# Kernel optimization log

Measured on AMD Instinct MI355X. Metric: run time of the kernel, lower is better.

Reference implementation:

```python
import jax, jax.numpy as jnp
import numpy as np

N_NODES = 100000
N_EDGES = 3200000
D_IN = 512
D_OUT = 256


def setup_inputs() -> dict:
    key = jax.random.key(0)
    k1, k2, k3, k4, k5 = jax.random.split(key, 5)
    x = jax.random.normal(k1, (N_NODES, D_IN), dtype=jnp.float32)
    edge_row = jax.random.randint(k2, (N_EDGES,), 0, N_NODES, dtype=jnp.int32)
    edge_col = jax.random.randint(k3, (N_EDGES,), 0, N_NODES, dtype=jnp.int32)
    edge_vals = jax.random.uniform(k4, (N_EDGES,), dtype=jnp.float32)
    # glorot uniform for W, zeros for bias (as in the torch module)
    init_range = float(np.sqrt(6.0 / (D_IN + D_OUT)))
    W = jax.random.uniform(k5, (D_IN, D_OUT), minval=-init_range, maxval=init_range, dtype=jnp.float32)
    b = jnp.zeros((D_OUT,), dtype=jnp.float32)
    return {"x": x, "edge_row": edge_row, "edge_col": edge_col,
            "edge_vals": edge_vals, "W": W, "b": b}


def reference(x, edge_row, edge_col, edge_vals, W, b):
    # dropout p=0 -> identity; feature transform
    pre_sup = x @ W                                   # [N, D_OUT]
    # SpMM: out[i] = sum_{e: row[e]==i} vals[e] * pre_sup[col[e]]
    gathered = pre_sup[edge_col] * edge_vals[:, None]  # [E, D_OUT]
    agg = jax.ops.segment_sum(gathered, edge_row, num_segments=N_NODES)
    out = agg + b
    # F.normalize(p=2, dim=0): L2-normalize each column over the node dim
    col_norm = jnp.sqrt(jnp.sum(out * out, axis=0, keepdims=True))
    out = out / jnp.maximum(col_norm, 1e-12)
    return jax.nn.softplus(out)
```

## Files before the change

### kernel.cpp

```cpp
#include <hip/hip_runtime.h>
#include <math.h>

#define N_NODES 100000
#define N_EDGES 3200000
#define D_IN 512
#define D_OUT 256
#define NBUK 391
#define LDA 40
#define NREP 8

typedef unsigned short ushort_t;
typedef unsigned int uint_t;

using f32x4 = __attribute__((ext_vector_type(4))) float;
using s16x8 = __attribute__((ext_vector_type(8))) short;
using u32x4 = __attribute__((ext_vector_type(4))) uint_t;

__device__ __forceinline__ ushort_t f2bf(float f) {
    union { float f; uint_t u; } v; v.f = f;
    uint_t r = v.u + 0x7FFFu + ((v.u >> 16) & 1u);
    return (ushort_t)(r >> 16);
}
__device__ __forceinline__ float bf2f(uint_t u) {
    union { uint_t u; float f; } v; v.u = u << 16;
    return v.f;
}

__global__ __launch_bounds__(256) void cvt_w(const float* __restrict__ W,
                                             ushort_t* __restrict__ Wt) {
    int idx = blockIdx.x * 256 + threadIdx.x;
    int k = idx >> 8, n = idx & 255;
    Wt[(size_t)n * D_IN + k] = f2bf(W[idx]);
}

__global__ __launch_bounds__(256) void gemm_xw(const float* __restrict__ X,
                                               const ushort_t* __restrict__ Wt,
                                               ushort_t* __restrict__ P) {
    __shared__ ushort_t As[128 * LDA];
    __shared__ ushort_t Bs[128 * LDA];
    const int tid = threadIdx.x;
    const int m0 = blockIdx.y * 128;
    const int wave = tid >> 6, lane = tid & 63;
    const int quad = lane >> 4, r16 = lane & 15;
    const int wm = (wave >> 1) * 64, wn = (wave & 1) * 64;

    for (int nt = 0; nt < 2; ++nt) {
        const int n0 = nt * 128;
        f32x4 acc[4][4] = {};

        for (int k0 = 0; k0 < D_IN; k0 += 32) {
#pragma unroll
            for (int it = 0; it < 2; ++it) {
                int f = tid + it * 256;
                int row = f >> 2, kc = (f & 3) * 8;
                int grow = m0 + row;
                s16x8 av = {};
                if (grow < N_NODES) {
                    const float* xp = X + (size_t)grow * D_IN + k0 + kc;
                    f32x4 v0 = *(const f32x4*)(xp);
                    f32x4 v1 = *(const f32x4*)(xp + 4);
                    av[0] = (short)f2bf(v0[0]); av[1] = (short)f2bf(v0[1]);
                    av[2] = (short)f2bf(v0[2]); av[3] = (short)f2bf(v0[3]);
                    av[4] = (short)f2bf(v1[0]); av[5] = (short)f2bf(v1[1]);
                    av[6] = (short)f2bf(v1[2]); av[7] = (short)f2bf(v1[3]);
                }
                *(s16x8*)(&As[row * LDA + kc]) = av;
                s16x8 bv = *(const s16x8*)(Wt + (size_t)(n0 + row) * D_IN + k0 + kc);
                *(s16x8*)(&Bs[row * LDA + kc]) = bv;
            }
            __syncthreads();

            s16x8 a[4], b[4];
#pragma unroll
            for (int i = 0; i < 4; ++i)
                a[i] = *(const s16x8*)(&As[(wm + i * 16 + r16) * LDA + quad * 8]);
#pragma unroll
            for (int j = 0; j < 4; ++j)
                b[j] = *(const s16x8*)(&Bs[(wn + j * 16 + r16) * LDA + quad * 8]);
#pragma unroll
            for (int i = 0; i < 4; ++i)
#pragma unroll
                for (int j = 0; j < 4; ++j)
                    acc[i][j] = __builtin_amdgcn_mfma_f32_16x16x32_bf16(a[i], b[j], acc[i][j], 0, 0, 0);
            __syncthreads();
        }

#pragma unroll
        for (int i = 0; i < 4; ++i) {
#pragma unroll
            for (int rr = 0; rr < 4; ++rr) {
                int grow = m0 + wm + i * 16 + quad * 4 + rr;
                if (grow >= N_NODES) continue;
#pragma unroll
                for (int j = 0; j < 4; ++j) {
                    int gcol = n0 + wn + j * 16 + r16;
                    P[(size_t)grow * D_OUT + gcol] = f2bf(acc[i][j][rr]);
                }
            }
        }
    }
}

__global__ __launch_bounds__(256) void bhist(const int* __restrict__ erow,
                                             int* __restrict__ bcnt) {
    __shared__ int l[NBUK];
    for (int b = threadIdx.x; b < NBUK; b += 256) l[b] = 0;
    __syncthreads();
    int base = blockIdx.x * 4096;
#pragma unroll
    for (int i = 0; i < 16; ++i) {
        int e = base + i * 256 + threadIdx.x;
        if (e < N_EDGES) atomicAdd(&l[erow[e] >> 8], 1);
    }
    __syncthreads();
    for (int b = threadIdx.x; b < NBUK; b += 256)
        if (l[b]) atomicAdd(&bcnt[b], l[b]);
}

__global__ void bscan(const int* __restrict__ bcnt, int* __restrict__ bbase,
                      int* __restrict__ bcursor, int* __restrict__ rstart) {
    __shared__ int sc[512];
    int t = threadIdx.x;
    int v = (t < NBUK) ? bcnt[t] : 0;
    sc[t] = v;
    __syncthreads();
    for (int off = 1; off < 512; off <<= 1) {
        int x = (t >= off) ? sc[t - off] : 0;
        __syncthreads();
        sc[t] += x;
        __syncthreads();
    }
    if (t < NBUK) { int excl = sc[t] - v; bbase[t] = excl; bcursor[t] = excl; }
    if (t == 0) { bbase[NBUK] = N_EDGES; rstart[N_NODES] = N_EDGES; }
}

__global__ __launch_bounds__(256) void bucket_scatter(const int* __restrict__ erow,
                                                      const int* __restrict__ ecol,
                                                      const float* __restrict__ eval,
                                                      int* __restrict__ bcursor,
                                                      uint2* __restrict__ bkt) {
    __shared__ int lcnt[NBUK];
    __shared__ int lbase[NBUK];
    const int t = threadIdx.x;
    for (int b = t; b < NBUK; b += 256) lcnt[b] = 0;
    __syncthreads();
    const int base = blockIdx.x * 4096;
#pragma unroll
    for (int i = 0; i < 16; ++i) {
        int e = base + i * 256 + t;
        if (e < N_EDGES) atomicAdd(&lcnt[erow[e] >> 8], 1);
    }
    __syncthreads();
    for (int b = t; b < NBUK; b += 256) {
        int c = lcnt[b];
        if (c) lbase[b] = atomicAdd(&bcursor[b], c);
        lcnt[b] = 0;
    }
    __syncthreads();
#pragma unroll
    for (int i = 0; i < 16; ++i) {
        int e = base + i * 256 + t;
        if (e < N_EDGES) {
            int r = erow[e];
            int b = r >> 8;
            int off = atomicAdd(&lcnt[b], 1);
            uint2 p;
            p.x = ((uint_t)(r & 255) << 17) | (uint_t)ecol[e];
            p.y = __float_as_uint(eval[e]);
            bkt[lbase[b] + off] = p;
        }
    }
}

__global__ __launch_bounds__(256) void csr_build(const uint2* __restrict__ bkt,
                                                 const int* __restrict__ bbase,
                                                 int* __restrict__ rstart,
                                                 uint2* __restrict__ csr) {
    __shared__ int hcnt[256];
    __shared__ int sc[256];
    __shared__ int cur[256];
    const int t = threadIdx.x, b = blockIdx.x;
    const int beg = bbase[b], end = bbase[b + 1];
    hcnt[t] = 0;
    __syncthreads();
    for (int i = beg + t; i < end; i += 256)
        atomicAdd(&hcnt[bkt[i].x >> 17], 1);
    __syncthreads();
    int v = hcnt[t];
    sc[t] = v;
    __syncthreads();
    for (int off = 1; off < 256; off <<= 1) {
        int x = (t >= off) ? sc[t - off] : 0;
        __syncthreads();
        sc[t] += x;
        __syncthreads();
    }
    int excl = sc[t] - v;
    int row = b * 256 + t;
    if (row < N_NODES) rstart[row] = beg + excl;
    cur[t] = excl;
    __syncthreads();
    for (int i = beg + t; i < end; i += 256) {
        uint2 u = bkt[i];
        int lr = u.x >> 17;
        int off = atomicAdd(&cur[lr], 1);
        uint2 o;
        o.x = u.x & 0x1FFFFu;
        o.y = u.y;
        csr[beg + off] = o;
    }
}

__global__ __launch_bounds__(256) void spmm_kernel(const uint2* __restrict__ csr,
                                                   const int* __restrict__ row_start,
                                                   const ushort_t* __restrict__ pre,
                                                   const float* __restrict__ bias,
                                                   float* __restrict__ out,
                                                   float* __restrict__ colsq) {
    __shared__ uint2 epairs[4][64];
    __shared__ float lcq[256];
    const int wv   = threadIdx.x >> 6;
    const int lane = threadIdx.x & 63;
    const int half = lane >> 5;
    const int l32  = lane & 31;
    const int node = blockIdx.x * 4 + wv;

    lcq[threadIdx.x] = 0.f;
    __syncthreads();

    const int beg = row_start[node], end = row_start[node + 1];

    float a0 = 0.f, a1 = 0.f, a2 = 0.f, a3 = 0.f;
    float a4 = 0.f, a5 = 0.f, a6 = 0.f, a7 = 0.f;

    for (int base = beg; base < end; base += 64) {
        const int cnt = min(end - base, 64);
        uint2 p0;
        p0.x = 0u; p0.y = 0u;
        if (lane < cnt) p0 = csr[base + lane];
        epairs[wv][lane] = p0;

        const int iters = (cnt + 7) >> 3;
        for (int it = 0; it < iters; ++it) {
            const int e0 = it * 8 + half;
            uint2 q0 = epairs[wv][e0 + 0];
            uint2 q1 = epairs[wv][e0 + 2];
            uint2 q2 = epairs[wv][e0 + 4];
            uint2 q3 = epairs[wv][e0 + 6];

            u32x4 g0 = *(const u32x4*)(pre + (((size_t)q0.x) << 8) + l32 * 8);
            u32x4 g1 = *(const u32x4*)(pre + (((size_t)q1.x) << 8) + l32 * 8);
            u32x4 g2 = *(const u32x4*)(pre + (((size_t)q2.x) << 8) + l32 * 8);
            u32x4 g3 = *(const u32x4*)(pre + (((size_t)q3.x) << 8) + l32 * 8);

            const float w0 = __uint_as_float(q0.y);
            const float w1 = __uint_as_float(q1.y);
            const float w2 = __uint_as_float(q2.y);
            const float w3 = __uint_as_float(q3.y);

            a0 = fmaf(w0, bf2f(g0[0] & 0xFFFFu), a0);
            a1 = fmaf(w0, bf2f(g0[0] >> 16),     a1);
            a2 = fmaf(w0, bf2f(g0[1] & 0xFFFFu), a2);
            a3 = fmaf(w0, bf2f(g0[1] >> 16),     a3);
            a4 = fmaf(w0, bf2f(g0[2] & 0xFFFFu), a4);
            a5 = fmaf(w0, bf2f(g0[2] >> 16),     a5);
            a6 = fmaf(w0, bf2f(g0[3] & 0xFFFFu), a6);
            a7 = fmaf(w0, bf2f(g0[3] >> 16),     a7);

            a0 = fmaf(w1, bf2f(g1[0] & 0xFFFFu), a0);
            a1 = fmaf(w1, bf2f(g1[0] >> 16),     a1);
            a2 = fmaf(w1, bf2f(g1[1] & 0xFFFFu), a2);
            a3 = fmaf(w1, bf2f(g1[1] >> 16),     a3);
            a4 = fmaf(w1, bf2f(g1[2] & 0xFFFFu), a4);
            a5 = fmaf(w1, bf2f(g1[2] >> 16),     a5);
            a6 = fmaf(w1, bf2f(g1[3] & 0xFFFFu), a6);
            a7 = fmaf(w1, bf2f(g1[3] >> 16),     a7);

            a0 = fmaf(w2, bf2f(g2[0] & 0xFFFFu), a0);
            a1 = fmaf(w2, bf2f(g2[0] >> 16),     a1);
            a2 = fmaf(w2, bf2f(g2[1] & 0xFFFFu), a2);
            a3 = fmaf(w2, bf2f(g2[1] >> 16),     a3);
            a4 = fmaf(w2, bf2f(g2[2] & 0xFFFFu), a4);
            a5 = fmaf(w2, bf2f(g2[2] >> 16),     a5);
            a6 = fmaf(w2, bf2f(g2[3] & 0xFFFFu), a6);
            a7 = fmaf(w2, bf2f(g2[3] >> 16),     a7);

            a0 = fmaf(w3, bf2f(g3[0] & 0xFFFFu), a0);
            a1 = fmaf(w3, bf2f(g3[0] >> 16),     a1);
            a2 = fmaf(w3, bf2f(g3[1] & 0xFFFFu), a2);
            a3 = fmaf(w3, bf2f(g3[1] >> 16),     a3);
            a4 = fmaf(w3, bf2f(g3[2] & 0xFFFFu), a4);
            a5 = fmaf(w3, bf2f(g3[2] >> 16),     a5);
            a6 = fmaf(w3, bf2f(g3[3] & 0xFFFFu), a6);
            a7 = fmaf(w3, bf2f(g3[3] >> 16),     a7);
        }
    }

    a0 += __shfl_xor(a0, 32);
    a1 += __shfl_xor(a1, 32);
    a2 += __shfl_xor(a2, 32);
    a3 += __shfl_xor(a3, 32);
    a4 += __shfl_xor(a4, 32);
    a5 += __shfl_xor(a5, 32);
    a6 += __shfl_xor(a6, 32);
    a7 += __shfl_xor(a7, 32);

    const int fbase = l32 * 8 + half * 4;
    const float* bp = bias + fbase;
    float s0 = half ? a4 : a0;
    float s1 = half ? a5 : a1;
    float s2 = half ? a6 : a2;
    float s3 = half ? a7 : a3;
    f32x4 o;
    o[0] = s0 + bp[0]; o[1] = s1 + bp[1]; o[2] = s2 + bp[2]; o[3] = s3 + bp[3];
    *(f32x4*)(out + (size_t)node * D_OUT + fbase) = o;

    atomicAdd(&lcq[fbase + 0], o[0] * o[0]);
    atomicAdd(&lcq[fbase + 1], o[1] * o[1]);
    atomicAdd(&lcq[fbase + 2], o[2] * o[2]);
    atomicAdd(&lcq[fbase + 3], o[3] * o[3]);
    __syncthreads();
    float c = lcq[threadIdx.x];
    if (c != 0.f)
        atomicAdd(&colsq[(blockIdx.x & (NREP - 1)) * 256 + threadIdx.x], c);
}

__global__ __launch_bounds__(256) void finalize_kernel(float* __restrict__ out,
                                                       const float* __restrict__ colsq) {
    __shared__ float inv[256];
    const int t = threadIdx.x;
    float s = 0.f;
#pragma unroll
    for (int r = 0; r < NREP; ++r) s += colsq[r * 256 + t];
    float n = sqrtf(s);
    inv[t] = 1.0f / fmaxf(n, 1e-12f);
    __syncthreads();
    const size_t total4 = (size_t)N_NODES * D_OUT / 4;
    for (size_t i = (size_t)blockIdx.x * 256 + t; i < total4; i += (size_t)gridDim.x * 256) {
        f32x4 v = ((const f32x4*)out)[i];
        int fbase = (int)((i * 4) & (D_OUT - 1));
        f32x4 o;
#pragma unroll
        for (int c = 0; c < 4; ++c) {
            float x = v[c] * inv[fbase + c];
            float tt = __expf(x);
            float y = __logf(1.0f + tt);
            o[c] = (x > 20.f) ? x : y;
        }
        ((f32x4*)out)[i] = o;
    }
}

extern "C" void kernel_launch(void* const* d_in, const int* in_sizes, int n_in,
                              void* d_out, int out_size, void* d_ws, size_t ws_size,
                              hipStream_t stream) {
    const float* x    = (const float*)d_in[0];
    const int*   erow = (const int*)d_in[1];
    const int*   ecol = (const int*)d_in[2];
    const float* eval = (const float*)d_in[3];
    const float* W    = (const float*)d_in[4];
    const float* b    = (const float*)d_in[5];
    float* out = (float*)d_out;
    char* ws = (char*)d_ws;

    uint2*    bkt     = (uint2*)   (ws + 0);
    ushort_t* pre     = (ushort_t*)(ws + 0);
    uint2*    csr     = (uint2*)   (ws + 51200000);
    int*      rstart  = (int*)     (ws + 76800000);
    float*    colsq   = (float*)   (ws + 77200016);
    int*      bcnt    = (int*)     (ws + 77208208);
    int*      bbase   = (int*)     (ws + 77209776);
    int*      bcursor = (int*)     (ws + 77211344);
    ushort_t* Wt      = (ushort_t*)(ws + 77212928);

    (void)hipMemsetAsync(bcnt, 0, NBUK * sizeof(int), stream);
    (void)hipMemsetAsync(colsq, 0, NREP * D_OUT * sizeof(float), stream);

    bhist<<<782, 256, 0, stream>>>(erow, bcnt);
    bscan<<<1, 512, 0, stream>>>(bcnt, bbase, bcursor, rstart);
    bucket_scatter<<<782, 256, 0, stream>>>(erow, ecol, eval, bcursor, bkt);
    csr_build<<<NBUK, 256, 0, stream>>>(bkt, bbase, rstart, csr);
    cvt_w<<<512, 256, 0, stream>>>(W, Wt);
    gemm_xw<<<dim3(1, 782), 256, 0, stream>>>(x, Wt, pre);
    spmm_kernel<<<N_NODES / 4, 256, 0, stream>>>(csr, rstart, pre, b, out, colsq);
    finalize_kernel<<<1024, 256, 0, stream>>>(out, colsq);
}
```

Before: 845.3 us.

## Widen GEMM tile to full output width and batch four nodes per SpMM wave

The GEMM now computes all 256 output columns per block in a single pass, so each X tile is loaded and converted to bf16 once instead of twice. This doubles the accumulator registers per thread and the B shared-memory tile. The SpMM kernel now has each wave process four nodes in sequence and keeps the column sum-of-squares in registers. This cuts shared and global atomics by a factor of four and reduces the block count. The trade-offs are higher register pressure in the GEMM and fewer blocks to balance irregular row lengths in the SpMM.

Result: no change. 840.0 us (-0.6%).

```diff
diff --git a/kernel.cpp b/kernel.cpp
--- a/kernel.cpp
+++ b/kernel.cpp
@@ -37,65 +37,67 @@
                                                const ushort_t* __restrict__ Wt,
                                                ushort_t* __restrict__ P) {
     __shared__ ushort_t As[128 * LDA];
-    __shared__ ushort_t Bs[128 * LDA];
+    __shared__ ushort_t Bs[256 * LDA];
     const int tid = threadIdx.x;
-    const int m0 = blockIdx.y * 128;
+    const int m0 = blockIdx.x * 128;
     const int wave = tid >> 6, lane = tid & 63;
     const int quad = lane >> 4, r16 = lane & 15;
-    const int wm = (wave >> 1) * 64, wn = (wave & 1) * 64;
-
-    for (int nt = 0; nt < 2; ++nt) {
-        const int n0 = nt * 128;
-        f32x4 acc[4][4] = {};
-
-        for (int k0 = 0; k0 < D_IN; k0 += 32) {
-#pragma unroll
-            for (int it = 0; it < 2; ++it) {
-                int f = tid + it * 256;
-                int row = f >> 2, kc = (f & 3) * 8;
-                int grow = m0 + row;
-                s16x8 av = {};
-                if (grow < N_NODES) {
-                    const float* xp = X + (size_t)grow * D_IN + k0 + kc;
-                    f32x4 v0 = *(const f32x4*)(xp);
-                    f32x4 v1 = *(const f32x4*)(xp + 4);
-                    av[0] = (short)f2bf(v0[0]); av[1] = (short)f2bf(v0[1]);
-                    av[2] = (short)f2bf(v0[2]); av[3] = (short)f2bf(v0[3]);
-                    av[4] = (short)f2bf(v1[0]); av[5] = (short)f2bf(v1[1]);
-                    av[6] = (short)f2bf(v1[2]); av[7] = (short)f2bf(v1[3]);
-                }
-                *(s16x8*)(&As[row * LDA + kc]) = av;
-                s16x8 bv = *(const s16x8*)(Wt + (size_t)(n0 + row) * D_IN + k0 + kc);
-                *(s16x8*)(&Bs[row * LDA + kc]) = bv;
+    const int wm = (wave >> 1) * 64;
+    const int wn = (wave & 1) * 128;
+
+    f32x4 acc[4][8] = {};
+
+    for (int k0 = 0; k0 < D_IN; k0 += 32) {
+#pragma unroll
+        for (int it = 0; it < 2; ++it) {
+            int f = tid + it * 256;
+            int row = f >> 2, kc = (f & 3) * 8;
+            int grow = m0 + row;
+            s16x8 av = {};
+            if (grow < N_NODES) {
+                const float* xp = X + (size_t)grow * D_IN + k0 + kc;
+                f32x4 v0 = *(const f32x4*)(xp);
+                f32x4 v1 = *(const f32x4*)(xp + 4);
+                av[0] = (short)f2bf(v0[0]); av[1] = (short)f2bf(v0[1]);
+                av[2] = (short)f2bf(v0[2]); av[3] = (short)f2bf(v0[3]);
+                av[4] = (short)f2bf(v1[0]); av[5] = (short)f2bf(v1[1]);
+                av[6] = (short)f2bf(v1[2]); av[7] = (short)f2bf(v1[3]);
             }
-            __syncthreads();
-
-            s16x8 a[4], b[4];
+            *(s16x8*)(&As[row * LDA + kc]) = av;
+        }
+#pragma unroll
+        for (int it = 0; it < 4; ++it) {
+            int f = tid + it * 256;
+            int row = f >> 2, kc = (f & 3) * 8;
+            s16x8 bv = *(const s16x8*)(Wt + (size_t)row * D_IN + k0 + kc);
+            *(s16x8*)(&Bs[row * LDA + kc]) = bv;
+        }
+        __syncthreads();
+
+        s16x8 a[4];
+#pragma unroll
+        for (int i = 0; i < 4; ++i)
+            a[i] = *(const s16x8*)(&As[(wm + i * 16 + r16) * LDA + quad * 8]);
+#pragma unroll
+        for (int j = 0; j < 8; ++j) {
+            s16x8 b = *(const s16x8*)(&Bs[(wn + j * 16 + r16) * LDA + quad * 8]);
 #pragma unroll
             for (int i = 0; i < 4; ++i)
-                a[i] = *(const s16x8*)(&As[(wm + i * 16 + r16) * LDA + quad * 8]);
-#pragma unroll
-            for (int j = 0; j < 4; ++j)
-                b[j] = *(const s16x8*)(&Bs[(wn + j * 16 + r16) * LDA + quad * 8]);
-#pragma unroll
-            for (int i = 0; i < 4; ++i)
-#pragma unroll
-                for (int j = 0; j < 4; ++j)
-                    acc[i][j] = __builtin_amdgcn_mfma_f32_16x16x32_bf16(a[i], b[j], acc[i][j], 0, 0, 0);
-            __syncthreads();
-        }
-
-#pragma unroll
-        for (int i = 0; i < 4; ++i) {
-#pragma unroll
-            for (int rr = 0; rr < 4; ++rr) {
-                int grow = m0 + wm + i * 16 + quad * 4 + rr;
-                if (grow >= N_NODES) continue;
-#pragma unroll
-                for (int j = 0; j < 4; ++j) {
-                    int gcol = n0 + wn + j * 16 + r16;
-                    P[(size_t)grow * D_OUT + gcol] = f2bf(acc[i][j][rr]);
-                }
+                acc[i][j] = __builtin_amdgcn_mfma_f32_16x16x32_bf16(a[i], b, acc[i][j], 0, 0, 0);
+        }
+        __syncthreads();
+    }
+
+#pragma unroll
+    for (int i = 0; i < 4; ++i) {
+#pragma unroll
+        for (int rr = 0; rr < 4; ++rr) {
+            int grow = m0 + wm + i * 16 + quad * 4 + rr;
+            if (grow >= N_NODES) continue;
+#pragma unroll
+            for (int j = 0; j < 8; ++j) {
+                int gcol = wn + j * 16 + r16;
+                P[(size_t)grow * D_OUT + gcol] = f2bf(acc[i][j][rr]);
             }
         }
     }
@@ -223,106 +225,115 @@
     const int lane = threadIdx.x & 63;
     const int half = lane >> 5;
     const int l32  = lane & 31;
-    const int node = blockIdx.x * 4 + wv;
+    const int fbase = l32 * 8 + half * 4;
 
     lcq[threadIdx.x] = 0.f;
     __syncthreads();
 
-    const int beg = row_start[node], end = row_start[node + 1];
-
-    float a0 = 0.f, a1 = 0.f, a2 = 0.f, a3 = 0.f;
-    float a4 = 0.f, a5 = 0.f, a6 = 0.f, a7 = 0.f;
-
-    for (int base = beg; base < end; base += 64) {
-        const int cnt = min(end - base, 64);
-        uint2 p0;
-        p0.x = 0u; p0.y = 0u;
-        if (lane < cnt) p0 = csr[base + lane];
-        epairs[wv][lane] = p0;
-
-        const int iters = (cnt + 7) >> 3;
-        for (int it = 0; it < iters; ++it) {
-            const int e0 = it * 8 + half;
-            uint2 q0 = epairs[wv][e0 + 0];
-            uint2 q1 = epairs[wv][e0 + 2];
-            uint2 q2 = epairs[wv][e0 + 4];
-            uint2 q3 = epairs[wv][e0 + 6];
-
-            u32x4 g0 = *(const u32x4*)(pre + (((size_t)q0.x) << 8) + l32 * 8);
-            u32x4 g1 = *(const u32x4*)(pre + (((size_t)q1.x) << 8) + l32 * 8);
-            u32x4 g2 = *(const u32x4*)(pre + (((size_t)q2.x) << 8) + l32 * 8);
-            u32x4 g3 = *(const u32x4*)(pre + (((size_t)q3.x) << 8) + l32 * 8);
-
-            const float w0 = __uint_as_float(q0.y);
-            const float w1 = __uint_as_float(q1.y);
-            const float w2 = __uint_as_float(q2.y);
-            const float w3 = __uint_as_float(q3.y);
-
-            a0 = fmaf(w0, bf2f(g0[0] & 0xFFFFu), a0);
-            a1 = fmaf(w0, bf2f(g0[0] >> 16),     a1);
-            a2 = fmaf(w0, bf2f(g0[1] & 0xFFFFu), a2);
-            a3 = fmaf(w0, bf2f(g0[1] >> 16),     a3);
-            a4 = fmaf(w0, bf2f(g0[2] & 0xFFFFu), a4);
-            a5 = fmaf(w0, bf2f(g0[2] >> 16),     a5);
-            a6 = fmaf(w0, bf2f(g0[3] & 0xFFFFu), a6);
-            a7 = fmaf(w0, bf2f(g0[3] >> 16),     a7);
-
-            a0 = fmaf(w1, bf2f(g1[0] & 0xFFFFu), a0);
-            a1 = fmaf(w1, bf2f(g1[0] >> 16),     a1);
-            a2 = fmaf(w1, bf2f(g1[1] & 0xFFFFu), a2);
-            a3 = fmaf(w1, bf2f(g1[1] >> 16),     a3);
-            a4 = fmaf(w1, bf2f(g1[2] & 0xFFFFu), a4);
-            a5 = fmaf(w1, bf2f(g1[2] >> 16),     a5);
-            a6 = fmaf(w1, bf2f(g1[3] & 0xFFFFu), a6);
-            a7 = fmaf(w1, bf2f(g1[3] >> 16),     a7);
-
-            a0 = fmaf(w2, bf2f(g2[0] & 0xFFFFu), a0);
-            a1 = fmaf(w2, bf2f(g2[0] >> 16),     a1);
-            a2 = fmaf(w2, bf2f(g2[1] & 0xFFFFu), a2);
-            a3 = fmaf(w2, bf2f(g2[1] >> 16),     a3);
-            a4 = fmaf(w2, bf2f(g2[2] & 0xFFFFu), a4);
-            a5 = fmaf(w2, bf2f(g2[2] >> 16),     a5);
-            a6 = fmaf(w2, bf2f(g2[3] & 0xFFFFu), a6);
-            a7 = fmaf(w2, bf2f(g2[3] >> 16),     a7);
-
-            a0 = fmaf(w3, bf2f(g3[0] & 0xFFFFu), a0);
-            a1 = fmaf(w3, bf2f(g3[0] >> 16),     a1);
-            a2 = fmaf(w3, bf2f(g3[1] & 0xFFFFu), a2);
-            a3 = fmaf(w3, bf2f(g3[1] >> 16),     a3);
-            a4 = fmaf(w3, bf2f(g3[2] & 0xFFFFu), a4);
-            a5 = fmaf(w3, bf2f(g3[2] >> 16),     a5);
-            a6 = fmaf(w3, bf2f(g3[3] & 0xFFFFu), a6);
-            a7 = fmaf(w3, bf2f(g3[3] >> 16),     a7);
-        }
-    }
-
-    a0 += __shfl_xor(a0, 32);
-    a1 += __shfl_xor(a1, 32);
-    a2 += __shfl_xor(a2, 32);
-    a3 += __shfl_xor(a3, 32);
-    a4 += __shfl_xor(a4, 32);
-    a5 += __shfl_xor(a5, 32);
-    a6 += __shfl_xor(a6, 32);
-    a7 += __shfl_xor(a7, 32);
-
-    const int fbase = l32 * 8 + half * 4;
     const float* bp = bias + fbase;
-    float s0 = half ? a4 : a0;
-    float s1 = half ? a5 : a1;
-    float s2 = half ? a6 : a2;
-    float s3 = half ? a7 : a3;
-    f32x4 o;
-    o[0] = s0 + bp[0]; o[1] = s1 + bp[1]; o[2] = s2 + bp[2]; o[3] = s3 + bp[3];
-    *(f32x4*)(out + (size_t)node * D_OUT + fbase) = o;
-
-    atomicAdd(&lcq[fbase + 0], o[0] * o[0]);
-    atomicAdd(&lcq[fbase + 1], o[1] * o[1]);
-    atomicAdd(&lcq[fbase + 2], o[2] * o[2]);
-    atomicAdd(&lcq[fbase + 3], o[3] * o[3]);
-    __syncthreads();
-    float c = lcq[threadIdx.x];
-    if (c != 0.f)
-        atomicAdd(&colsq[(blockIdx.x & (NREP - 1)) * 256 + threadIdx.x], c);
+    const float b0 = bp[0], b1 = bp[1], b2 = bp[2], b3 = bp[3];
+    float c0 = 0.f, c1 = 0.f, c2 = 0.f, c3 = 0.f;
+
+#pragma unroll 1
+    for (int s = 0; s < 4; ++s) {
+        const int node = blockIdx.x * 16 + wv * 4 + s;
+        const int beg = row_start[node], end = row_start[node + 1];
+
+        float a0 = 0.f, a1 = 0.f, a2 = 0.f, a3 = 0.f;
+        float a4 = 0.f, a5 = 0.f, a6 = 0.f, a7 = 0.f;
+
+        for (int base = beg; base < end; base += 64) {
+            const int cnt = min(end - base, 64);
+            uint2 p0;
+            p0.x = 0u; p0.y = 0u;
+            if (lane < cnt) p0 = csr[base + lane];
+            epairs[wv][lane] = p0;
+
+            const int iters = (cnt + 7) >> 3;
+            for (int it = 0; it < iters; ++it) {
+                const int e0 = it * 8 + half;
+                uint2 q0 = epairs[wv][e0 + 0];
+                uint2 q1 = epairs[wv][e0 + 2];
+                uint2 q2 = epairs[wv][e0 + 4];
+                uint2 q3 = epairs[wv][e0 + 6];
+
+                u32x4 g0 = *(const u32x4*)(pre + (((size_t)q0.x) << 8) + l32 * 8);
+                u32x4 g1 = *(const u32x4*)(pre + (((size_t)q1.x) << 8) + l32 * 8);
+                u32x4 g2 = *(const u32x4*)(pre + (((size_t)q2.x) << 8) + l32 * 8);
+                u32x4 g3 = *(const u32x4*)(pre + (((size_t)q3.x) << 8) + l32 * 8);
+
+                const float w0 = __uint_as_float(q0.y);
+                const float w1 = __uint_as_float(q1.y);
+                const float w2 = __uint_as_float(q2.y);
+                const float w3 = __uint_as_float(q3.y);
+
+                a0 = fmaf(w0, bf2f(g0[0] & 0xFFFFu), a0);
+                a1 = fmaf(w0, bf2f(g0[0] >> 16),     a1);
+                a2 = fmaf(w0, bf2f(g0[1] & 0xFFFFu), a2);
+                a3 = fmaf(w0, bf2f(g0[1] >> 16),     a3);
+                a4 = fmaf(w0, bf2f(g0[2] & 0xFFFFu), a4);
+                a5 = fmaf(w0, bf2f(g0[2] >> 16),     a5);
+                a6 = fmaf(w0, bf2f(g0[3] & 0xFFFFu), a6);
+                a7 = fmaf(w0, bf2f(g0[3] >> 16),     a7);
+
+                a0 = fmaf(w1, bf2f(g1[0] & 0xFFFFu), a0);
+                a1 = fmaf(w1, bf2f(g1[0] >> 16),     a1);
+                a2 = fmaf(w1, bf2f(g1[1] & 0xFFFFu), a2);
+                a3 = fmaf(w1, bf2f(g1[1] >> 16),     a3);
+                a4 = fmaf(w1, bf2f(g1[2] & 0xFFFFu), a4);
+                a5 = fmaf(w1, bf2f(g1[2] >> 16),     a5);
+                a6 = fmaf(w1, bf2f(g1[3] & 0xFFFFu), a6);
+                a7 = fmaf(w1, bf2f(g1[3] >> 16),     a7);
+
+                a0 = fmaf(w2, bf2f(g2[0] & 0xFFFFu), a0);
+                a1 = fmaf(w2, bf2f(g2[0] >> 16),     a1);
+                a2 = fmaf(w2, bf2f(g2[1] & 0xFFFFu), a2);
+                a3 = fmaf(w2, bf2f(g2[1] >> 16),     a3);
+                a4 = fmaf(w2, bf2f(g2[2] & 0xFFFFu), a4);
+                a5 = fmaf(w2, bf2f(g2[2] >> 16),     a5);
+                a6 = fmaf(w2, bf2f(g2[3] & 0xFFFFu), a6);
+                a7 = fmaf(w2, bf2f(g2[3] >> 16),     a7);
+
+                a0 = fmaf(w3, bf2f(g3[0] & 0xFFFFu), a0);
+                a1 = fmaf(w3, bf2f(g3[0] >> 16),     a1);
+                a2 = fmaf(w3, bf2f(g3[1] & 0xFFFFu), a2);
+                a3 = fmaf(w3, bf2f(g3[1] >> 16),     a3);
+                a4 = fmaf(w3, bf2f(g3[2] & 0xFFFFu), a4);
+                a5 = fmaf(w3, bf2f(g3[2] >> 16),     a5);
+                a6 = fmaf(w3, bf2f(g3[3] & 0xFFFFu), a6);
+                a7 = fmaf(w3, bf2f(g3[3] >> 16),     a7);
+            }
+        }
+
+        a0 += __shfl_xor(a0, 32);
+        a1 += __shfl_xor(a1, 32);
+        a2 += __shfl_xor(a2, 32);
+        a3 += __shfl_xor(a3, 32);
+        a4 += __shfl_xor(a4, 32);
+        a5 += __shfl_xor(a5, 32);
+        a6 += __shfl_xor(a6, 32);
+        a7 += __shfl_xor(a7, 32);
+
+        float s0 = half ? a4 : a0;
+        float s1 = half ? a5 : a1;
+        float s2 = half ? a6 : a2;
+        float s3 = half ? a7 : a3;
+        f32x4 o;
+        o[0] = s0 + b0; o[1] = s1 + b1; o[2] = s2 + b2; o[3] = s3 + b3;
+        *(f32x4*)(out + (size_t)node * D_OUT + fbase) = o;
+
+        c0 = fmaf(o[0], o[0], c0);
+        c1 = fmaf(o[1], o[1], c1);
+        c2 = fmaf(o[2], o[2], c2);
+        c3 = fmaf(o[3], o[3], c3);
+    }
+
+    atomicAdd(&lcq[fbase + 0], c0);
+    atomicAdd(&lcq[fbase + 1], c1);
+    atomicAdd(&lcq[fbase + 2], c2);
+    atomicAdd(&lcq[fbase + 3], c3);
+    __syncthreads();
+    atomicAdd(&colsq[(blockIdx.x & (NREP - 1)) * 256 + threadIdx.x], lcq[threadIdx.x]);
 }
 
 __global__ __launch_bounds__(256) void finalize_kernel(float* __restrict__ out,
@@ -381,7 +392,7 @@
     bucket_scatter<<<782, 256, 0, stream>>>(erow, ecol, eval, bcursor, bkt);
     csr_build<<<NBUK, 256, 0, stream>>>(bkt, bbase, rstart, csr);
     cvt_w<<<512, 256, 0, stream>>>(W, Wt);
-    gemm_xw<<<dim3(1, 782), 256, 0, stream>>>(x, Wt, pre);
-    spmm_kernel<<<N_NODES / 4, 256, 0, stream>>>(csr, rstart, pre, b, out, colsq);
+    gemm_xw<<<782, 256, 0, stream>>>(x, Wt, pre);
+    spmm_kernel<<<N_NODES / 16, 256, 0, stream>>>(csr, rstart, pre, b, out, colsq);
     finalize_kernel<<<1024, 256, 0, stream>>>(out, colsq);
 }
```
